# Optimization experiments

Hardware: AMD Instinct MI355X
Metric: run time of the kernel (lower is better)

## Reference

```python
import jax, jax.numpy as jnp
import numpy as np

DIM = 1024
NUM_HEADS = 16
HEAD_DIM = DIM // NUM_HEADS
SCALING = HEAD_DIM ** (-0.5)


def setup_inputs() -> dict:
    key = jax.random.key(0)
    ks = jax.random.split(key, 9)
    B, S = 2, 2048
    s = DIM ** -0.5  # ~ torch Linear init scale
    inp = {
        "x": jax.random.normal(ks[0], (B, S, DIM), dtype=jnp.float32),
        "wq": jax.random.uniform(ks[1], (DIM, DIM), jnp.float32, -s, s),
        "bq": jax.random.uniform(ks[2], (DIM,), jnp.float32, -s, s),
        "wk": jax.random.uniform(ks[3], (DIM, DIM), jnp.float32, -s, s),
        "bk": jax.random.uniform(ks[4], (DIM,), jnp.float32, -s, s),
        "wv": jax.random.uniform(ks[5], (DIM, DIM), jnp.float32, -s, s),
        "bv": jax.random.uniform(ks[6], (DIM,), jnp.float32, -s, s),
        "wo": jax.random.uniform(ks[7], (DIM, DIM), jnp.float32, -s, s),
        "bo": jax.random.uniform(ks[8], (DIM,), jnp.float32, -s, s),
    }
    return inp


def reference(x, wq, bq, wk, bk, wv, bv, wo, bo):
    B, S, D = x.shape
    # projections (weights stored [out,in] like torch Linear -> x @ W.T + b)
    q = (x @ wq.T + bq).reshape(B, S, NUM_HEADS, HEAD_DIM)
    k = (x @ wk.T + bk).reshape(B, S, NUM_HEADS, HEAD_DIM)
    v = (x @ wv.T + bv).reshape(B, S, NUM_HEADS, HEAD_DIM)
    # [B,H,S,S] scores, scaled
    scores = jnp.einsum("bqhd,bkhd->bhqk", q, k) * SCALING
    attn = jax.nn.softmax(scores, axis=-1)
    # dropout p=0.0 (eval): identity
    out = jnp.einsum("bhqk,bkhd->bqhd", attn, v).reshape(B, S, D)
    return out @ wo.T + bo
```

## Files before the change

kernel.cpp:

```cpp
#include <hip/hip_runtime.h>

#define DIM 1024
#define NHEADS 16
#define HDIM 64
#define BATCH 2
#define SEQ 2048
#define MTOT (BATCH*SEQ)
#define QSCALE 0.18033688011112042f
#define XN ((size_t)MTOT*DIM)
#define WN ((size_t)DIM*DIM)

typedef __attribute__((ext_vector_type(8))) short short8;
typedef __attribute__((ext_vector_type(4))) float f32x4;
typedef __attribute__((ext_vector_type(16))) float f32x16;
typedef __attribute__((ext_vector_type(2))) int int2v;

static __device__ __forceinline__ unsigned short bf16rne(float f) {
    unsigned u = __builtin_bit_cast(unsigned, f);
    return (unsigned short)((u + 0x7fffu + ((u >> 16) & 1u)) >> 16);
}

static __device__ __forceinline__ void gld16(const void* g, void* l) {
    __builtin_amdgcn_global_load_lds((const __attribute__((address_space(1))) void*)g,
                                     (__attribute__((address_space(3))) void*)l, 16, 0, 0);
}

static __device__ __forceinline__ f32x16 mfma32(short8 a, short8 b, f32x16 c) {
    return __builtin_amdgcn_mfma_f32_32x32x16_bf16(a, b, c, 0, 0, 0);
}

__global__ __launch_bounds__(256)
void prep(const float* __restrict__ x, const float* __restrict__ wq, const float* __restrict__ wk,
          const float* __restrict__ wv, const float* __restrict__ wo, unsigned short* __restrict__ dst)
{
    const size_t i = ((size_t)blockIdx.x*256 + threadIdx.x)*8;
    const float* s; size_t o;
    if (i < XN)           { s = x;  o = i; }
    else if (i < XN+WN)   { s = wq; o = i - XN; }
    else if (i < XN+2*WN) { s = wk; o = i - XN - WN; }
    else if (i < XN+3*WN) { s = wv; o = i - XN - 2*WN; }
    else                  { s = wo; o = i - XN - 3*WN; }
    float4 a = *(const float4*)(s + o);
    float4 b = *(const float4*)(s + o + 4);
    uint4 w;
    w.x = (unsigned)bf16rne(a.x) | ((unsigned)bf16rne(a.y) << 16);
    w.y = (unsigned)bf16rne(a.z) | ((unsigned)bf16rne(a.w) << 16);
    w.z = (unsigned)bf16rne(b.x) | ((unsigned)bf16rne(b.y) << 16);
    w.w = (unsigned)bf16rne(b.z) | ((unsigned)bf16rne(b.w) << 16);
    *(uint4*)&dst[i] = w;
}

__global__ __launch_bounds__(256)
void gemm_qkv(const unsigned short* __restrict__ A,
              const unsigned short* __restrict__ W0, const unsigned short* __restrict__ W1,
              const unsigned short* __restrict__ W2,
              const float* __restrict__ b0, const float* __restrict__ b1, const float* __restrict__ b2,
              unsigned short* __restrict__ o0, unsigned short* __restrict__ o1, unsigned short* __restrict__ o2)
{
    __shared__ __align__(16) unsigned short smem[24576];
    #define AS(s) (smem + (s)*4096)
    #define BS(s) (smem + 12288 + (s)*4096)
    const int t = threadIdx.x, wid = t >> 6, lane = t & 63;
    const int lr = lane & 15, lg = lane >> 4;
    const int bid = blockIdx.y * 24 + blockIdx.x;
    const int swz = (bid & 7) * 96 + (bid >> 3);
    const int sx = swz % 24, sy = swz / 24;
    const int widx = sx >> 3;
    const int n0 = (sx & 7) << 7;
    const int m0 = sy << 7;
    const unsigned short* W = widx == 0 ? W0 : (widx == 1 ? W1 : W2);
    const float* bias        = widx == 0 ? b0 : (widx == 1 ? b1 : b2);

    const int wm = wid >> 1, wn = wid & 1;
    const int f0 = 2*wid, f1 = f0 + 1;
    const unsigned short* Ag0 = A + (size_t)(m0 + f0*16 + lr)*DIM + lg*8;
    const unsigned short* Ag1 = A + (size_t)(m0 + f1*16 + lr)*DIM + lg*8;
    const unsigned short* Bg0 = W + (size_t)(n0 + f0*16 + lr)*DIM + lg*8;
    const unsigned short* Bg1 = W + (size_t)(n0 + f1*16 + lr)*DIM + lg*8;

    auto stage = [&](int tt, int slot) {
        const int ko = tt * 32;
        gld16(Ag0 + ko, AS(slot) + f0*512); gld16(Ag1 + ko, AS(slot) + f1*512);
        gld16(Bg0 + ko, BS(slot) + f0*512); gld16(Bg1 + ko, BS(slot) + f1*512);
    };

    f32x4 acc[4][4] = {};
    stage(0, 0); stage(1, 1);
    int c0 = 0, c1 = 1, c2 = 2;

    for (int it = 0; it < DIM/32; ++it) {
        if (it < DIM/32 - 2) { asm volatile("s_waitcnt vmcnt(4)" ::: "memory"); }
        else                 { asm volatile("s_waitcnt vmcnt(0)" ::: "memory"); }
        __builtin_amdgcn_s_barrier();
        short8 af[4], bf[4];
        #pragma unroll
        for (int i = 0; i < 4; ++i) af[i] = *(const short8*)(AS(c0) + (wm*4+i)*512 + lane*8);
        #pragma unroll
        for (int i = 0; i < 4; ++i) bf[i] = *(const short8*)(BS(c0) + (wn*4+i)*512 + lane*8);
        if (it + 2 < DIM/32) stage(it + 2, c2);
        __builtin_amdgcn_s_setprio(1);
        #pragma unroll
        for (int mb = 0; mb < 4; ++mb)
            #pragma unroll
            for (int nb = 0; nb < 4; ++nb)
                acc[mb][nb] = __builtin_amdgcn_mfma_f32_16x16x32_bf16(af[mb], bf[nb], acc[mb][nb], 0, 0, 0);
        __builtin_amdgcn_s_setprio(0);
        const int tmp = c0; c0 = c1; c1 = c2; c2 = tmp;
    }

    if (widx == 0) {
        #pragma unroll
        for (int nb = 0; nb < 4; ++nb) {
            const int col = n0 + wn*64 + nb*16 + lr;
            const float bv = bias[col];
            #pragma unroll
            for (int mb = 0; mb < 4; ++mb) {
                #pragma unroll
                for (int j = 0; j < 4; ++j) {
                    const int row = m0 + wm*64 + mb*16 + lg*4 + j;
                    o0[(size_t)row*DIM + col] = bf16rne((acc[mb][nb][j] + bv) * QSCALE);
                }
            }
        }
    } else {
        unsigned short* outp = (widx == 1) ? o1 : o2;
        const int isV = (widx == 2);
        __syncthreads();
        unsigned short (*tile)[136] = (unsigned short (*)[136])smem;
        #pragma unroll
        for (int nb = 0; nb < 4; ++nb) {
            const int col = wn*64 + nb*16 + lr;
            const float bv = bias[n0 + col];
            #pragma unroll
            for (int mb = 0; mb < 4; ++mb) {
                #pragma unroll
                for (int j = 0; j < 4; ++j)
                    tile[wm*64 + mb*16 + lg*4 + j][col] = bf16rne(acc[mb][nb][j] + bv);
            }
        }
        __syncthreads();
        const int bb  = m0 >> 11;
        const int kt0 = (m0 & (SEQ-1)) >> 6;
        const int hh0 = n0 >> 6;
        #pragma unroll
        for (int shot = 0; shot < 8; ++shot) {
            const int idx = t + shot*256;
            const int tid = idx >> 9;
            const int fr  = (idx >> 6) & 7;
            const int ln  = idx & 63;
            const int ktl = tid & 1, hhl = tid >> 1;
            short8 ov;
            if (isV) {
                const int r0 = ktl*64 + (fr & 3)*16 + (ln >> 5)*8;
                const int c  = hhl*64 + (fr >> 2)*32 + (ln & 31);
                #pragma unroll
                for (int e = 0; e < 8; ++e) ov[e] = (short)tile[r0 + e][c];
            } else {
                const int r  = ktl*64 + (fr >> 2)*32 + (ln & 31);
                const int cc = hhl*64 + (fr & 3)*16 + (ln >> 5)*8;
                ov = *(const short8*)&tile[r][cc];
            }
            unsigned short* dst = outp
                + ((size_t)((bb*NHEADS + hh0 + hhl)*32 + kt0 + ktl))*4096 + fr*512 + ln*8;
            *(short8*)dst = ov;
        }
    }
    #undef AS
    #undef BS
}

__global__ __launch_bounds__(256)
void gemm_o(const unsigned short* __restrict__ A, const unsigned short* __restrict__ W,
            const float* __restrict__ bias, float* __restrict__ fo)
{
    __shared__ __align__(16) unsigned short As[3][2048];
    __shared__ __align__(16) unsigned short Bs[3][4096];
    const int t = threadIdx.x, wid = t >> 6, lane = t & 63;
    const int lr = lane & 15, lg = lane >> 4;
    const int bid = blockIdx.y * 8 + blockIdx.x;
    const int swz = (bid & 7) * 64 + (bid >> 3);
    const int n0 = (swz & 7) << 7;
    const int m0 = (swz >> 3) << 6;
    const int wm = wid >> 1, wn = wid & 1;

    const int fa = wid;
    const int g0 = 2*wid, g1 = g0 + 1;
    const unsigned short* Ag  = A + (size_t)(m0 + fa*16 + lr)*DIM + lg*8;
    const unsigned short* Bg0 = W + (size_t)(n0 + g0*16 + lr)*DIM + lg*8;
    const unsigned short* Bg1 = W + (size_t)(n0 + g1*16 + lr)*DIM + lg*8;

    auto stage = [&](int tt, int slot) {
        const int ko = tt * 32;
        gld16(Ag + ko, &As[slot][fa*512]);
        gld16(Bg0 + ko, &Bs[slot][g0*512]); gld16(Bg1 + ko, &Bs[slot][g1*512]);
    };

    f32x4 acc[2][4] = {};
    stage(0, 0); stage(1, 1);
    int c0 = 0, c1 = 1, c2 = 2;

    for (int it = 0; it < DIM/32; ++it) {
        if (it < DIM/32 - 2) { asm volatile("s_waitcnt vmcnt(3)" ::: "memory"); }
        else                 { asm volatile("s_waitcnt vmcnt(0)" ::: "memory"); }
        __builtin_amdgcn_s_barrier();
        short8 af[2], bf[4];
        #pragma unroll
        for (int i = 0; i < 2; ++i) af[i] = *(const short8*)&As[c0][(wm*2+i)*512 + lane*8];
        #pragma unroll
        for (int i = 0; i < 4; ++i) bf[i] = *(const short8*)&Bs[c0][(wn*4+i)*512 + lane*8];
        if (it + 2 < DIM/32) stage(it + 2, c2);
        __builtin_amdgcn_s_setprio(1);
        #pragma unroll
        for (int mb = 0; mb < 2; ++mb)
            #pragma unroll
            for (int nb = 0; nb < 4; ++nb)
                acc[mb][nb] = __builtin_amdgcn_mfma_f32_16x16x32_bf16(af[mb], bf[nb], acc[mb][nb], 0, 0, 0);
        __builtin_amdgcn_s_setprio(0);
        const int tmp = c0; c0 = c1; c1 = c2; c2 = tmp;
    }

    #pragma unroll
    for (int nb = 0; nb < 4; ++nb) {
        const int col = n0 + wn*64 + nb*16 + lr;
        const float bv = bias[col];
        #pragma unroll
        for (int mb = 0; mb < 2; ++mb) {
            #pragma unroll
            for (int j = 0; j < 4; ++j) {
                const int row = m0 + wm*32 + mb*16 + lg*4 + j;
                fo[(size_t)row*DIM + col] = acc[mb][nb][j] + bv;
            }
        }
    }
}

struct PA2 { short8 p[2]; };

static __device__ __forceinline__ PA2 smpack32(const f32x16& s0, float& lsum) {
    float rsum = 0.f;
    unsigned pw0[4][2];
    #pragma unroll
    for (int r1 = 0; r1 < 4; ++r1)
        #pragma unroll
        for (int tt = 0; tt < 2; ++tt) {
            float pa_ = __builtin_amdgcn_exp2f(s0[4*r1+2*tt]);
            float pb_ = __builtin_amdgcn_exp2f(s0[4*r1+2*tt+1]);
            rsum += pa_ + pb_;
            asm("v_cvt_pk_bf16_f32 %0, %1, %2" : "=v"(pw0[r1][tt]) : "v"(pa_), "v"(pb_));
        }
    rsum += __shfl_xor(rsum, 32);
    lsum += rsum;
    PA2 r;
    #pragma unroll
    for (int ss = 0; ss < 2; ++ss) {
        union { short8 s8; unsigned u[4]; } pu;
        #pragma unroll
        for (int tt = 0; tt < 2; ++tt) {
            int2v sw = __builtin_amdgcn_permlane32_swap(
                (int)pw0[2*ss][tt], (int)pw0[2*ss+1][tt], false, false);
            pu.u[tt]     = (unsigned)sw[0];
            pu.u[2 + tt] = (unsigned)sw[1];
        }
        r.p[ss] = pu.s8;
    }
    return r;
}

__global__ __launch_bounds__(512)
void attn_mfma3(const unsigned short* __restrict__ Q, const unsigned short* __restrict__ Kp,
                const unsigned short* __restrict__ Vp, unsigned short* __restrict__ O)
{
    __shared__ __align__(16) unsigned char smem[67584];
    unsigned short* KsB = (unsigned short*)smem;
    unsigned short* VsB = (unsigned short*)(smem + 32768);
    float* cb = (float*)smem;

    const int t = threadIdx.x, wid = t >> 6, lane = t & 63;
    const int l31 = lane & 31, h = lane >> 5;
    const int g = wid >> 1;
    const int kh = wid & 1;
    const int bid = blockIdx.y * 8 + blockIdx.x;
    const int swz = (bid & 7) * 32 + (bid >> 3);
    const int qt = swz & 7, bh = swz >> 3;
    const int b = bh >> 4, hh = bh & 15;
    const size_t qkbase = (size_t)b*SEQ*DIM + (size_t)hh*HDIM;
    const unsigned short* Qb = Q + qkbase;
    unsigned short*       Ob = O + qkbase;
    const int q0 = qt*256 + g*64;

    short8 qfA[4], qfB[4];
    #pragma unroll
    for (int ds = 0; ds < 4; ++ds) {
        qfA[ds] = *(const short8*)&Qb[(size_t)(q0 + l31)*DIM + ds*16 + h*8];
        qfB[ds] = *(const short8*)&Qb[(size_t)(q0 + 32 + l31)*DIM + ds*16 + h*8];
    }

    const unsigned short* Kg = Kp + (size_t)bh*32*4096 + wid*512 + lane*8;
    const unsigned short* Vg = Vp + (size_t)bh*32*4096 + wid*512 + lane*8;

    auto stage = [&](int tn) {
        const size_t ko = (size_t)tn * 4096;
        const int bb = tn & 3;
        gld16(Kg + ko, KsB + bb*4096 + wid*512);
        gld16(Vg + ko, VsB + bb*4096 + wid*512);
    };

    f32x16 ctxA0 = {}, ctxA1 = {}, ctxB0 = {}, ctxB1 = {};
    float lsumA = 0.0f, lsumB = 0.0f;

    stage(0); stage(1);

    const int NW = SEQ/128;
    for (int w = 0; w < NW; ++w) {
        const int t0 = 2*w;
        const int ba = t0 & 3, bb2 = (t0+1) & 3;
        const bool more = (w + 1 < NW);

        if (more) { asm volatile("s_waitcnt vmcnt(2)" ::: "memory"); }
        else      { asm volatile("s_waitcnt vmcnt(0)" ::: "memory"); }
        __builtin_amdgcn_s_barrier();
        if (more) stage(t0 + 2);

        f32x16 sA = {}, sB = {};
        __builtin_amdgcn_s_setprio(1);
        #pragma unroll
        for (int ds = 0; ds < 4; ++ds) {
            short8 kf = *(const short8*)(KsB + ba*4096 + (4*kh + ds)*512 + lane*8);
            sA = mfma32(kf, qfA[ds], sA);
            sB = mfma32(kf, qfB[ds], sB);
        }
        __builtin_amdgcn_s_setprio(0);

        PA2 paA = smpack32(sA, lsumA);
        PA2 paB = smpack32(sB, lsumB);

        if (more) { asm volatile("s_waitcnt vmcnt(2)" ::: "memory"); }
        else      { asm volatile("s_waitcnt vmcnt(0)" ::: "memory"); }
        __builtin_amdgcn_s_barrier();
        if (more) stage(t0 + 3);

        f32x16 rA = {}, rB = {};
        __builtin_amdgcn_s_setprio(1);
        #pragma unroll
        for (int ds = 0; ds < 4; ++ds) {
            short8 kf = *(const short8*)(KsB + bb2*4096 + (4*kh + ds)*512 + lane*8);
            rA = mfma32(kf, qfA[ds], rA);
            rB = mfma32(kf, qfB[ds], rB);
        }
        #pragma unroll
        for (int ls = 0; ls < 2; ++ls) {
            short8 vf0 = *(const short8*)(VsB + ba*4096 + (2*kh + ls)*512 + lane*8);
            short8 vf1 = *(const short8*)(VsB + ba*4096 + (4 + 2*kh + ls)*512 + lane*8);
            ctxA0 = mfma32(paA.p[ls], vf0, ctxA0);
            ctxA1 = mfma32(paA.p[ls], vf1, ctxA1);
            ctxB0 = mfma32(paB.p[ls], vf0, ctxB0);
            ctxB1 = mfma32(paB.p[ls], vf1, ctxB1);
        }
        __builtin_amdgcn_s_setprio(0);

        PA2 pbA = smpack32(rA, lsumA);
        PA2 pbB = smpack32(rB, lsumB);

        __builtin_amdgcn_s_setprio(1);
        #pragma unroll
        for (int ls = 0; ls < 2; ++ls) {
            short8 vf0 = *(const short8*)(VsB + bb2*4096 + (2*kh + ls)*512 + lane*8);
            short8 vf1 = *(const short8*)(VsB + bb2*4096 + (4 + 2*kh + ls)*512 + lane*8);
            ctxA0 = mfma32(pbA.p[ls], vf0, ctxA0);
            ctxA1 = mfma32(pbA.p[ls], vf1, ctxA1);
            ctxB0 = mfma32(pbB.p[ls], vf0, ctxB0);
            ctxB1 = mfma32(pbB.p[ls], vf1, ctxB1);
        }
        __builtin_amdgcn_s_setprio(0);
    }

    __syncthreads();
    if (kh == 1) {
        float* dst = cb + ((size_t)g*64 + lane)*66;
        #pragma unroll
        for (int r = 0; r < 16; ++r) {
            dst[r]      = ctxA0[r];
            dst[16 + r] = ctxA1[r];
            dst[32 + r] = ctxB0[r];
            dst[48 + r] = ctxB1[r];
        }
        dst[64] = lsumA;
        dst[65] = lsumB;
    }
    __syncthreads();
    if (kh == 0) {
        const float* src = cb + ((size_t)g*64 + lane)*66;
        #pragma unroll
        for (int r = 0; r < 16; ++r) {
            ctxA0[r] += src[r];
            ctxA1[r] += src[16 + r];
            ctxB0[r] += src[32 + r];
            ctxB1[r] += src[48 + r];
        }
        lsumA += src[64];
        lsumB += src[65];

        const float linvA = 1.0f / lsumA;
        const float linvB = 1.0f / lsumB;
        #pragma unroll
        for (int r = 0; r < 16; ++r) {
            const int qrow = (r&3) + 8*(r>>2) + 4*h;
            const float nmA = __shfl(linvA, qrow);
            const float nmB = __shfl(linvB, qrow);
            unsigned short* pA = &Ob[(size_t)(q0 + qrow)*DIM + l31];
            unsigned short* pB = &Ob[(size_t)(q0 + 32 + qrow)*DIM + l31];
            pA[0]  = bf16rne(ctxA0[r] * nmA);
            pA[32] = bf16rne(ctxA1[r] * nmA);
            pB[0]  = bf16rne(ctxB0[r] * nmB);
            pB[32] = bf16rne(ctxB1[r] * nmB);
        }
    }
}

extern "C" void kernel_launch(void* const* d_in, const int* in_sizes, int n_in,
                              void* d_out, int out_size, void* d_ws, size_t ws_size,
                              hipStream_t stream) {
    const float* x  = (const float*)d_in[0];
    const float* wq = (const float*)d_in[1];
    const float* bq = (const float*)d_in[2];
    const float* wk = (const float*)d_in[3];
    const float* bk = (const float*)d_in[4];
    const float* wv = (const float*)d_in[5];
    const float* bv = (const float*)d_in[6];
    const float* wo = (const float*)d_in[7];
    const float* bo = (const float*)d_in[8];
    float* out = (float*)d_out;

    unsigned short* Xb  = (unsigned short*)d_ws;
    unsigned short* Wqb = Xb  + XN;
    unsigned short* Wkb = Wqb + WN;
    unsigned short* Wvb = Wkb + WN;
    unsigned short* Wob = Wvb + WN;
    unsigned short* Qb  = Wob + WN;
    unsigned short* Kpb = Qb  + XN;
    unsigned short* Vpb = Kpb + XN;
    unsigned short* Cb  = Xb;

    prep<<<4096, 256, 0, stream>>>(x, wq, wk, wv, wo, Xb);

    gemm_qkv<<<dim3(24, 32), 256, 0, stream>>>(Xb, Wqb, Wkb, Wvb, bq, bk, bv, Qb, Kpb, Vpb);

    attn_mfma3<<<dim3(8, BATCH*NHEADS), 512, 0, stream>>>(Qb, Kpb, Vpb, Cb);

    gemm_o<<<dim3(8, 64), 256, 0, stream>>>(Cb, Wob, bo, out);
}
```

Measured before the change: 127.5 us.

## Load K/V tiles directly into registers instead of staging through LDS

The attention kernel no longer stages K and V tiles into shared memory with global_load_lds and barriers. Each wave now loads its own K/V fragments straight from global memory into registers, double-buffered across the two tiles per iteration, and prefetches the next tiles right after each use. This removes the LDS round trip and the per-tile block barriers. In exchange it increases VGPR pressure and makes each wave pay full global/L2 latency, and waves sharing a block now issue redundant K/V loads.

```diff
diff --git a/kernel.cpp b/kernel.cpp
--- a/kernel.cpp
+++ b/kernel.cpp
@@ -267,13 +267,10 @@
 }
 
 __global__ __launch_bounds__(512)
-void attn_mfma3(const unsigned short* __restrict__ Q, const unsigned short* __restrict__ Kp,
-                const unsigned short* __restrict__ Vp, unsigned short* __restrict__ O)
+void attn_reg(const unsigned short* __restrict__ Q, const unsigned short* __restrict__ Kp,
+              const unsigned short* __restrict__ Vp, unsigned short* __restrict__ O)
 {
-    __shared__ __align__(16) unsigned char smem[67584];
-    unsigned short* KsB = (unsigned short*)smem;
-    unsigned short* VsB = (unsigned short*)(smem + 32768);
-    float* cb = (float*)smem;
+    __shared__ float cb[4*64*66];
 
     const int t = threadIdx.x, wid = t >> 6, lane = t & 63;
     const int l31 = lane & 31, h = lane >> 5;
@@ -295,83 +292,77 @@
         qfB[ds] = *(const short8*)&Qb[(size_t)(q0 + 32 + l31)*DIM + ds*16 + h*8];
     }
 
-    const unsigned short* Kg = Kp + (size_t)bh*32*4096 + wid*512 + lane*8;
-    const unsigned short* Vg = Vp + (size_t)bh*32*4096 + wid*512 + lane*8;
-
-    auto stage = [&](int tn) {
+    const unsigned short* Kb = Kp + (size_t)bh*32*4096 + (4*kh)*512 + lane*8;
+    const unsigned short* Vb = Vp + (size_t)bh*32*4096 + (2*kh)*512 + lane*8;
+
+    auto loadK = [&](int tn, short8 k[4]) {
         const size_t ko = (size_t)tn * 4096;
-        const int bb = tn & 3;
-        gld16(Kg + ko, KsB + bb*4096 + wid*512);
-        gld16(Vg + ko, VsB + bb*4096 + wid*512);
+        #pragma unroll
+        for (int ds = 0; ds < 4; ++ds) k[ds] = *(const short8*)(Kb + ko + ds*512);
+    };
+    auto loadV = [&](int tn, short8 v[4]) {
+        const size_t ko = (size_t)tn * 4096;
+        #pragma unroll
+        for (int dh = 0; dh < 2; ++dh)
+            #pragma unroll
+            for (int ls = 0; ls < 2; ++ls) v[dh*2+ls] = *(const short8*)(Vb + ko + dh*2048 + ls*512);
     };
 
     f32x16 ctxA0 = {}, ctxA1 = {}, ctxB0 = {}, ctxB1 = {};
     float lsumA = 0.0f, lsumB = 0.0f;
 
-    stage(0); stage(1);
-
-    const int NW = SEQ/128;
-    for (int w = 0; w < NW; ++w) {
-        const int t0 = 2*w;
-        const int ba = t0 & 3, bb2 = (t0+1) & 3;
-        const bool more = (w + 1 < NW);
-
-        if (more) { asm volatile("s_waitcnt vmcnt(2)" ::: "memory"); }
-        else      { asm volatile("s_waitcnt vmcnt(0)" ::: "memory"); }
-        __builtin_amdgcn_s_barrier();
-        if (more) stage(t0 + 2);
+    short8 kA[4], vA[4], kB[4], vB[4];
+    loadK(0, kA); loadV(0, vA);
+    loadK(1, kB); loadV(1, vB);
+
+    #pragma unroll 1
+    for (int w = 0; w < SEQ/128; ++w) {
+        const int tn0 = (2*w + 2) & 31;
+        const int tn1 = (2*w + 3) & 31;
 
         f32x16 sA = {}, sB = {};
         __builtin_amdgcn_s_setprio(1);
         #pragma unroll
         for (int ds = 0; ds < 4; ++ds) {
-            short8 kf = *(const short8*)(KsB + ba*4096 + (4*kh + ds)*512 + lane*8);
-            sA = mfma32(kf, qfA[ds], sA);
-            sB = mfma32(kf, qfB[ds], sB);
-        }
-        __builtin_amdgcn_s_setprio(0);
-
+            sA = mfma32(kA[ds], qfA[ds], sA);
+            sB = mfma32(kA[ds], qfB[ds], sB);
+        }
+        __builtin_amdgcn_s_setprio(0);
+        loadK(tn0, kA);
         PA2 paA = smpack32(sA, lsumA);
         PA2 paB = smpack32(sB, lsumB);
-
-        if (more) { asm volatile("s_waitcnt vmcnt(2)" ::: "memory"); }
-        else      { asm volatile("s_waitcnt vmcnt(0)" ::: "memory"); }
-        __builtin_amdgcn_s_barrier();
-        if (more) stage(t0 + 3);
+        __builtin_amdgcn_s_setprio(1);
+        #pragma unroll
+        for (int ls = 0; ls < 2; ++ls) {
+            ctxA0 = mfma32(paA.p[ls], vA[ls],     ctxA0);
+            ctxA1 = mfma32(paA.p[ls], vA[2 + ls], ctxA1);
+            ctxB0 = mfma32(paB.p[ls], vA[ls],     ctxB0);
+            ctxB1 = mfma32(paB.p[ls], vA[2 + ls], ctxB1);
+        }
+        __builtin_amdgcn_s_setprio(0);
+        loadV(tn0, vA);
 
         f32x16 rA = {}, rB = {};
         __builtin_amdgcn_s_setprio(1);
         #pragma unroll
         for (int ds = 0; ds < 4; ++ds) {
-            short8 kf = *(const short8*)(KsB + bb2*4096 + (4*kh + ds)*512 + lane*8);
-            rA = mfma32(kf, qfA[ds], rA);
-            rB = mfma32(kf, qfB[ds], rB);
-        }
-        #pragma unroll
-        for (int ls = 0; ls < 2; ++ls) {
-            short8 vf0 = *(const short8*)(VsB + ba*4096 + (2*kh + ls)*512 + lane*8);
-            short8 vf1 = *(const short8*)(VsB + ba*4096 + (4 + 2*kh + ls)*512 + lane*8);
-            ctxA0 = mfma32(paA.p[ls], vf0, ctxA0);
-            ctxA1 = mfma32(paA.p[ls], vf1, ctxA1);
-            ctxB0 = mfma32(paB.p[ls], vf0, ctxB0);
-            ctxB1 = mfma32(paB.p[ls], vf1, ctxB1);
-        }
-        __builtin_amdgcn_s_setprio(0);
-
+            rA = mfma32(kB[ds], qfA[ds], rA);
+            rB = mfma32(kB[ds], qfB[ds], rB);
+        }
+        __builtin_amdgcn_s_setprio(0);
+        loadK(tn1, kB);
         PA2 pbA = smpack32(rA, lsumA);
         PA2 pbB = smpack32(rB, lsumB);
-
         __builtin_amdgcn_s_setprio(1);
         #pragma unroll
         for (int ls = 0; ls < 2; ++ls) {
-            short8 vf0 = *(const short8*)(VsB + bb2*4096 + (2*kh + ls)*512 + lane*8);
-            short8 vf1 = *(const short8*)(VsB + bb2*4096 + (4 + 2*kh + ls)*512 + lane*8);
-            ctxA0 = mfma32(pbA.p[ls], vf0, ctxA0);
-            ctxA1 = mfma32(pbA.p[ls], vf1, ctxA1);
-            ctxB0 = mfma32(pbB.p[ls], vf0, ctxB0);
-            ctxB1 = mfma32(pbB.p[ls], vf1, ctxB1);
-        }
-        __builtin_amdgcn_s_setprio(0);
+            ctxA0 = mfma32(pbA.p[ls], vB[ls],     ctxA0);
+            ctxA1 = mfma32(pbA.p[ls], vB[2 + ls], ctxA1);
+            ctxB0 = mfma32(pbB.p[ls], vB[ls],     ctxB0);
+            ctxB1 = mfma32(pbB.p[ls], vB[2 + ls], ctxB1);
+        }
+        __builtin_amdgcn_s_setprio(0);
+        loadV(tn1, vB);
     }
 
     __syncthreads();
@@ -445,7 +436,7 @@
 
     gemm_qkv<<<dim3(24, 32), 256, 0, stream>>>(Xb, Wqb, Wkb, Wvb, bq, bk, bv, Qb, Kpb, Vpb);
 
-    attn_mfma3<<<dim3(8, BATCH*NHEADS), 512, 0, stream>>>(Qb, Kpb, Vpb, Cb);
+    attn_reg<<<dim3(8, BATCH*NHEADS), 512, 0, stream>>>(Qb, Kpb, Vpb, Cb);
 
     gemm_o<<<dim3(8, 64), 256, 0, stream>>>(Cb, Wob, bo, out);
 }
```

Result: no change. 129.2 us (+1.3%).
